# Performance work log

Measured on AMD Instinct MI355X. Metric: run time of the kernel, lower is better.

The kernel has to match this reference:

```python
import jax, jax.numpy as jnp
import numpy as np

B, S, D = 2, 1024, 1024
N_HEADS = 16
R = 128
M = 8
N_NEURONS = 256


def group_gate(gate, n_basis):
    # gate: [B,S,N] -> [B,S,M], sum over consecutive groups, then normalize
    b, s, n = gate.shape
    gs = n // n_basis  # exact by construction (256/8)
    g = gate.reshape(b, s, n_basis, gs).sum(axis=-1)
    return g / (g.sum(axis=-1, keepdims=True) + 1e-8)


def feature_fn(x, neurons, weights):
    # x:[B,S,D], neurons:[M,D,R], weights:[B,S,M] -> h:[B,S,R]
    all_h = jnp.einsum('bsd,mdr->bsmr', x, neurons)
    return jnp.einsum('bsmr,bsm->bsr', all_h, weights)


def restore_fn(h, neurons, weights):
    # h:[B,S,R], neurons:[M,R,D], weights:[B,S,M] -> [B,S,D]
    pre = jnp.einsum('bsr,bsm->bsmr', h, weights)
    return jnp.einsum('bsmr,mrd->bsd', pre, neurons)


def setup_inputs() -> dict:
    key = jax.random.key(0)
    ks = jax.random.split(key, 9)
    sc = 0.02
    return {
        'x': jax.random.normal(ks[0], (B, S, D), jnp.float32),
        'qk_f': jax.random.normal(ks[1], (M, D, R), jnp.float32) * sc,
        'qk_r': jax.random.normal(ks[2], (M, R, D), jnp.float32) * sc,
        'v_f': jax.random.normal(ks[3], (M, D, R), jnp.float32) * sc,
        'v_r': jax.random.normal(ks[4], (M, R, D), jnp.float32) * sc,
        'Wg_q': jax.random.normal(ks[5], (D, N_NEURONS), jnp.float32) * sc,
        'Wg_k': jax.random.normal(ks[6], (D, N_NEURONS), jnp.float32) * sc,
        'Wg_v': jax.random.normal(ks[7], (D, N_NEURONS), jnp.float32) * sc,
        'W_O': jax.random.normal(ks[8], (D, D), jnp.float32) * sc,
    }


def reference(x, qk_f, qk_r, v_f, v_r, Wg_q, Wg_k, Wg_v, W_O):
    # Router gates (softmax over neuron dim), then grouped per basis
    g_Q = jax.nn.softmax(jnp.einsum('bsd,dn->bsn', x, Wg_q), axis=-1)
    g_K = jax.nn.softmax(jnp.einsum('bsd,dn->bsn', x, Wg_k), axis=-1)
    g_V = jax.nn.softmax(jnp.einsum('bsd,dn->bsn', x, Wg_v), axis=-1)
    gQ_b = group_gate(g_Q, M)
    gK_b = group_gate(g_K, M)
    gV_b = group_gate(g_V, M)

    Q = restore_fn(feature_fn(x, qk_f, gQ_b), qk_r, gQ_b)
    K = restore_fn(feature_fn(x, qk_f, gK_b), qk_r, gK_b)
    V = restore_fn(feature_fn(x, v_f, gV_b), v_r, gV_b)

    d_head = D // N_HEADS
    Q = Q.reshape(B, S, N_HEADS, d_head).transpose(0, 2, 1, 3)
    K = K.reshape(B, S, N_HEADS, d_head).transpose(0, 2, 1, 3)
    V = V.reshape(B, S, N_HEADS, d_head).transpose(0, 2, 1, 3)

    scale = jnp.sqrt(jnp.float32(d_head))
    scores = jnp.einsum('bhsd,bhtd->bhst', Q, K) / scale
    causal = jnp.tril(jnp.ones((S, S), dtype=jnp.bool_))
    scores = jnp.where(causal, scores, jnp.finfo(scores.dtype).min)
    attn_w = jax.nn.softmax(scores, axis=-1)
    out = jnp.einsum('bhst,bhtd->bhsd', attn_w, V)
    out = out.transpose(0, 2, 1, 3).reshape(B, S, D)
    out = jnp.einsum('bsd,de->bse', out, W_O)
    return out
```

## Files before the change

### kernel.cpp

```cpp
#include <hip/hip_runtime.h>
#include <hip/hip_bf16.h>

#define BB 2
#define SS 1024
#define DD 1024
#define NH 16
#define DH 64
#define MM 8
#define RR 128
#define NN 256
#define NT (BB*SS)

using bf16 = __hip_bfloat16;

typedef __attribute__((ext_vector_type(8))) short short8;
typedef __attribute__((ext_vector_type(4))) short short4v;
typedef __attribute__((ext_vector_type(4))) float f32x4;

__device__ __forceinline__ void stf(float* p, size_t i, float v) { p[i] = v; }
__device__ __forceinline__ void stf(bf16* p, size_t i, float v) { p[i] = __float2bfloat16(v); }

#define GLD16(g, l) __builtin_amdgcn_global_load_lds( \
    (const __attribute__((address_space(1))) void*)(g), \
    (__attribute__((address_space(3))) void*)(l), 16, 0, 0)

__device__ __forceinline__ short8 lds_load8(const short* p) {
    short4v a = *(const short4v*)p;
    short4v b = *(const short4v*)(p + 4);
    short8 r;
    r[0] = a[0]; r[1] = a[1]; r[2] = a[2]; r[3] = a[3];
    r[4] = b[0]; r[5] = b[1]; r[6] = b[2]; r[7] = b[3];
    return r;
}

template <typename TC>
__device__ __forceinline__ void gemm64_body(
    const bf16* __restrict__ A, const bf16* __restrict__ Bt, TC* __restrict__ C,
    int Kdim, int Nz, int m0, int n0, bf16* As, bf16* Bs) {
    const int tid = threadIdx.x;
    const int wave = tid >> 6, lane = tid & 63;
    const int quad = lane >> 4, l15 = lane & 15;
    const int wr = wave >> 1, wc = wave & 1;

    f32x4 acc[2][4];
#pragma unroll
    for (int i = 0; i < 2; ++i)
#pragma unroll
        for (int j = 0; j < 4; ++j) acc[i][j] = (f32x4)0.f;

    for (int k0 = 0; k0 < Kdim; k0 += 64) {
        __syncthreads();
#pragma unroll
        for (int i = 0; i < 2; ++i) {
            const int L = i * 256 + wave * 64 + lane;
            const int row = L >> 3;
            const int gch = (L & 7) ^ ((row >> 1) & 7);
            GLD16(A + (size_t)(m0 + row) * Kdim + k0 + gch * 8, &As[(i * 256 + wave * 64) * 8]);
        }
#pragma unroll
        for (int i = 0; i < 4; ++i) {
            const int L = i * 256 + wave * 64 + lane;
            const int row = L >> 3;
            const int gch = (L & 7) ^ ((row >> 1) & 7);
            GLD16(Bt + (size_t)(n0 + row) * Kdim + k0 + gch * 8, &Bs[(i * 256 + wave * 64) * 8]);
        }
        __syncthreads();

#pragma unroll
        for (int kk = 0; kk < 2; ++kk) {
            short8 aF[2], bF[4];
#pragma unroll
            for (int bi = 0; bi < 2; ++bi) {
                int m = wr * 32 + bi * 16 + l15;
                int slot = (kk * 4 + quad) ^ ((m >> 1) & 7);
                aF[bi] = *(const short8*)&As[(m * 8 + slot) * 8];
            }
#pragma unroll
            for (int bj = 0; bj < 4; ++bj) {
                int n = wc * 64 + bj * 16 + l15;
                int slot = (kk * 4 + quad) ^ ((n >> 1) & 7);
                bF[bj] = *(const short8*)&Bs[(n * 8 + slot) * 8];
            }
#pragma unroll
            for (int bi = 0; bi < 2; ++bi)
#pragma unroll
                for (int bj = 0; bj < 4; ++bj)
                    acc[bi][bj] = __builtin_amdgcn_mfma_f32_16x16x32_bf16(aF[bi], bF[bj], acc[bi][bj], 0, 0, 0);
        }
    }

#pragma unroll
    for (int bi = 0; bi < 2; ++bi)
#pragma unroll
        for (int bj = 0; bj < 4; ++bj)
#pragma unroll
            for (int r = 0; r < 4; ++r) {
                int row = m0 + wr * 32 + bi * 16 + quad * 4 + r;
                int col = n0 + wc * 64 + bj * 16 + l15;
                stf(C, (size_t)row * Nz + col, acc[bi][bj][r]);
            }
}

struct GemmZ {
    const bf16* A[5];
    const bf16* Bt[5];
    void* C[5];
    int N[5];
};

__global__ __launch_bounds__(256) void mfma_proj(GemmZ P, int Kdim) {
    __shared__ bf16 As[64 * 64];
    __shared__ bf16 Bs[128 * 64];
    const int bidx = blockIdx.x;
    int z, xx, yy;
    if (bidx < 512) { z = bidx >> 8; int r = bidx & 255; yy = r >> 3; xx = r & 7; }
    else { int r = bidx - 512; z = 2 + r / 64; r = r % 64; yy = r >> 1; xx = r & 1; }
    gemm64_body<bf16>(P.A[z], P.Bt[z], (bf16*)P.C[z], Kdim, P.N[z], yy * 64, xx * 128, As, Bs);
}

__global__ __launch_bounds__(256) void mfma_restore(GemmZ P, int Kdim) {
    __shared__ bf16 As[64 * 64];
    __shared__ bf16 Bs[128 * 64];
    const int z = blockIdx.z;
    gemm64_body<bf16>(P.A[z], P.Bt[z], (bf16*)P.C[z], Kdim, P.N[z],
                      blockIdx.y * 64, blockIdx.x * 128, As, Bs);
}

__global__ __launch_bounds__(256) void mfma_gemm_64(
    const bf16* __restrict__ A, const bf16* __restrict__ Bt, float* __restrict__ C,
    int Kdim, int Ndim) {
    __shared__ bf16 As[64 * 64];
    __shared__ bf16 Bs[128 * 64];
    gemm64_body<float>(A, Bt, C, Kdim, Ndim, blockIdx.y * 64, blockIdx.x * 128, As, Bs);
}

struct ConvJobs {
    const float* src[9];
    bf16* dst[9];
    int K[9], R[9], G[9];
    int tEnd[9];
};

__global__ void convert_kernel(ConvJobs J) {
    __shared__ float tile[32][33];
    const int b = blockIdx.x;
    int j = 0;
    while (j < 8 && b >= J.tEnd[j]) ++j;
    const int local = b - (j > 0 ? J.tEnd[j - 1] : 0);
    const float* src = J.src[j];
    bf16* dst = J.dst[j];
    const int tid = threadIdx.x;

    if (J.G[j] == 0) {
        size_t base = (size_t)local * 4096 + (size_t)tid * 16;
        const float4* s4 = (const float4*)(src + base);
        short* d = (short*)(dst + base);
#pragma unroll
        for (int c = 0; c < 4; ++c) {
            float4 v = s4[c];
            short4v o;
            bf16 t0 = __float2bfloat16(v.x); o[0] = *(short*)&t0;
            bf16 t1 = __float2bfloat16(v.y); o[1] = *(short*)&t1;
            bf16 t2 = __float2bfloat16(v.z); o[2] = *(short*)&t2;
            bf16 t3 = __float2bfloat16(v.w); o[3] = *(short*)&t3;
            *(short4v*)(d + c * 4) = o;
        }
    } else {
        const int Kj = J.K[j], Rj = J.R[j];
        const int Rb = Rj >> 5, Kb = Kj >> 5;
        const int perG = Kb * Rb;
        const int g = local / perG;
        const int rem = local - g * perG;
        const int kb = rem / Rb, rb = rem - kb * Rb;
        const int tx = tid & 31, ty0 = tid >> 5;
        const float* s = src + ((size_t)(g * Kj + kb * 32) * Rj) + rb * 32 + tx;
#pragma unroll
        for (int p = 0; p < 4; ++p)
            tile[ty0 + p * 8][tx] = s[(size_t)(ty0 + p * 8) * Rj];
        __syncthreads();
        bf16* dd = dst + ((size_t)(g * Rj + rb * 32) * Kj) + kb * 32 + tx;
#pragma unroll
        for (int p = 0; p < 4; ++p)
            dd[(size_t)(ty0 + p * 8) * Kj] = __float2bfloat16(tile[tx][ty0 + p * 8]);
    }
}

__global__ void gate_combine(const bf16* __restrict__ logitsAll,
                             const bf16* __restrict__ allh,
                             bf16* __restrict__ preQ, bf16* __restrict__ preK,
                             bf16* __restrict__ preV) {
    const int t = blockIdx.x;
    const int n = threadIdx.x;
    const int wave = n >> 6, lane = n & 63;
    __shared__ float wred[3][4];
    __shared__ float sred[3][4];
    __shared__ float gred[3][8];

    float v[3], e[3];
#pragma unroll
    for (int z = 0; z < 3; ++z)
        v[z] = __bfloat162float(logitsAll[(size_t)z * NT * NN + (size_t)t * NN + n]);

    float mz[3];
#pragma unroll
    for (int z = 0; z < 3; ++z) {
        mz[z] = v[z];
#pragma unroll
        for (int off = 1; off <= 32; off <<= 1)
            mz[z] = fmaxf(mz[z], __shfl_xor(mz[z], off));
    }
    if (lane == 0) {
#pragma unroll
        for (int z = 0; z < 3; ++z) wred[z][wave] = mz[z];
    }
    __syncthreads();
    float gmax[3];
#pragma unroll
    for (int z = 0; z < 3; ++z)
        gmax[z] = fmaxf(fmaxf(wred[z][0], wred[z][1]), fmaxf(wred[z][2], wred[z][3]));

    float ws[3];
#pragma unroll
    for (int z = 0; z < 3; ++z) {
        e[z] = __expf(v[z] - gmax[z]);
        ws[z] = e[z];
#pragma unroll
        for (int off = 1; off <= 32; off <<= 1)
            ws[z] += __shfl_xor(ws[z], off);
    }
    if (lane == 0) {
#pragma unroll
        for (int z = 0; z < 3; ++z) sred[z][wave] = ws[z];
    }
    float gs[3];
#pragma unroll
    for (int z = 0; z < 3; ++z) {
        gs[z] = e[z];
#pragma unroll
        for (int off = 1; off <= 16; off <<= 1)
            gs[z] += __shfl_xor(gs[z], off);
    }
    __syncthreads();
    float total[3];
#pragma unroll
    for (int z = 0; z < 3; ++z)
        total[z] = sred[z][0] + sred[z][1] + sred[z][2] + sred[z][3];
    if ((n & 31) == 0) {
#pragma unroll
        for (int z = 0; z < 3; ++z) gred[z][n >> 5] = gs[z] / total[z];
    }
    __syncthreads();

    float gv[3][8];
#pragma unroll
    for (int z = 0; z < 3; ++z) {
        float tot = 0.f;
#pragma unroll
        for (int m = 0; m < 8; ++m) tot += gred[z][m];
        float inv = 1.0f / (tot + 1e-8f);
#pragma unroll
        for (int m = 0; m < 8; ++m) gv[z][m] = gred[z][m] * inv;
    }

    const int r0 = n & 127;
    const int half = n >> 7;
    const bf16* src_qk = allh + (size_t)t * 1024;
    const bf16* src_v  = allh + (size_t)NT * DD + (size_t)t * 1024;
    float hq = 0.f, hk = 0.f, hv = 0.f;
#pragma unroll
    for (int m = 0; m < 8; ++m) {
        float aqk = __bfloat162float(src_qk[m * 128 + r0]);
        float av  = __bfloat162float(src_v[m * 128 + r0]);
        hq += aqk * gv[0][m];
        hk += aqk * gv[1][m];
        hv += av  * gv[2][m];
    }
    __syncthreads();
#pragma unroll
    for (int mm = 0; mm < 4; ++mm) {
        int m = half * 4 + mm;
        size_t o = (size_t)t * 1024 + m * 128 + r0;
        preQ[o] = __float2bfloat16(hq * gv[0][m]);
        preK[o] = __float2bfloat16(hk * gv[1][m]);
        preV[o] = __float2bfloat16(hv * gv[2][m]);
    }
}

#define LDK 68

__global__ __launch_bounds__(256) void flash_attn_causal(
    const bf16* __restrict__ Q, const bf16* __restrict__ K,
    const bf16* __restrict__ V, bf16* __restrict__ out) {
    const int bx = blockIdx.x;
    const int qt = 15 - (bx >> 5);
    const int bh = bx & 31;
    const int b = bh >> 4;
    const int h = bh & 15;
    const int kt_hi = qt + 1;

    const int tid = threadIdx.x;
    const int wave = tid >> 6;
    const int lane = tid & 63;
    const int quad = lane >> 4;
    const int l15 = lane & 15;

    __shared__ short Ks[2][64 * 64];
    __shared__ short Vt[2][64 * LDK];
    __shared__ short Ps[4 * 16 * LDK];

    const int q_row = qt * 64 + wave * 16 + l15;
    const bf16* qptr = Q + (size_t)(b * SS + q_row) * DD + h * DH + quad * 8;
    short8 aq0 = *(const short8*)qptr;
    short8 aq1 = *(const short8*)(qptr + 32);

    const int krp = tid & 31;
    const int dhb = (tid >> 5) * 8;

    float m_r[4], l_r[4];
    f32x4 o[4];
#pragma unroll
    for (int r = 0; r < 4; ++r) { m_r[r] = -3.0e38f; l_r[r] = 0.f; }
#pragma unroll
    for (int cc = 0; cc < 4; ++cc) o[cc] = (f32x4)0.f;

    const float scale = 0.125f;

    {
#pragma unroll
        for (int i = 0; i < 2; ++i) {
            const int L = i * 256 + wave * 64 + lane;
            const int row = L >> 3;
            const int gch = (L & 7) ^ ((row >> 1) & 7);
            GLD16(K + (size_t)(b * SS + row) * DD + h * DH + gch * 8,
                  &Ks[0][(i * 256 + wave * 64) * 8]);
        }
        const bf16* s0 = V + (size_t)(b * SS + 2 * krp) * DD + h * DH + dhb;
        short8 r0 = *(const short8*)s0;
        short8 r1 = *(const short8*)(s0 + DD);
#pragma unroll
        for (int i = 0; i < 8; ++i) {
            unsigned int pk = (unsigned short)r0[i] | ((unsigned int)(unsigned short)r1[i] << 16);
            *(unsigned int*)&Vt[0][(dhb + i) * LDK + 2 * krp] = pk;
        }
        __syncthreads();
    }

    for (int kt = 0; kt < kt_hi; ++kt) {
        const int buf = kt & 1;
        const bool pf = (kt + 1 < kt_hi);
        short8 pr0, pr1;
        if (pf) {
#pragma unroll
            for (int i = 0; i < 2; ++i) {
                const int L = i * 256 + wave * 64 + lane;
                const int row = L >> 3;
                const int gch = (L & 7) ^ ((row >> 1) & 7);
                GLD16(K + (size_t)(b * SS + (kt + 1) * 64 + row) * DD + h * DH + gch * 8,
                      &Ks[buf ^ 1][(i * 256 + wave * 64) * 8]);
            }
            const bf16* s0 = V + (size_t)(b * SS + (kt + 1) * 64 + 2 * krp) * DD + h * DH + dhb;
            pr0 = *(const short8*)s0;
            pr1 = *(const short8*)(s0 + DD);
        }

        const short* KsB = Ks[buf];
        f32x4 s[4];
#pragma unroll
        for (int cc = 0; cc < 4; ++cc) {
            int n = cc * 16 + l15;
            int sl0 = quad ^ ((n >> 1) & 7);
            int sl1 = (quad + 4) ^ ((n >> 1) & 7);
            short8 bk0 = *(const short8*)&KsB[(n * 8 + sl0) * 8];
            short8 bk1 = *(const short8*)&KsB[(n * 8 + sl1) * 8];
            f32x4 acc = (f32x4)0.f;
            acc = __builtin_amdgcn_mfma_f32_16x16x32_bf16(aq0, bk0, acc, 0, 0, 0);
            acc = __builtin_amdgcn_mfma_f32_16x16x32_bf16(aq1, bk1, acc, 0, 0, 0);
            s[cc] = acc;
        }

        const bool diag = (kt == qt);
#pragma unroll
        for (int cc = 0; cc < 4; ++cc) {
#pragma unroll
            for (int r = 0; r < 4; ++r) {
                float v = s[cc][r] * scale;
                if (diag) {
                    int row_rel = wave * 16 + quad * 4 + r;
                    int col_rel = cc * 16 + l15;
                    if (col_rel > row_rel) v = -3.0e38f;
                }
                s[cc][r] = v;
            }
        }

        float p[4][4];
        float alpha[4];
#pragma unroll
        for (int r = 0; r < 4; ++r) {
            float mx = fmaxf(fmaxf(s[0][r], s[1][r]), fmaxf(s[2][r], s[3][r]));
            mx = fmaxf(mx, __shfl_xor(mx, 1));
            mx = fmaxf(mx, __shfl_xor(mx, 2));
            mx = fmaxf(mx, __shfl_xor(mx, 4));
            mx = fmaxf(mx, __shfl_xor(mx, 8));
            float new_m = fmaxf(m_r[r], mx);
            alpha[r] = __expf(m_r[r] - new_m);
            float rs = 0.f;
#pragma unroll
            for (int cc = 0; cc < 4; ++cc) {
                float e = __expf(s[cc][r] - new_m);
                p[cc][r] = e;
                rs += e;
            }
            rs += __shfl_xor(rs, 1);
            rs += __shfl_xor(rs, 2);
            rs += __shfl_xor(rs, 4);
            rs += __shfl_xor(rs, 8);
            l_r[r] = l_r[r] * alpha[r] + rs;
            m_r[r] = new_m;
        }
#pragma unroll
        for (int cc = 0; cc < 4; ++cc)
#pragma unroll
            for (int r = 0; r < 4; ++r) o[cc][r] *= alpha[r];

        short* pw = &Ps[wave * 16 * LDK];
#pragma unroll
        for (int cc = 0; cc < 4; ++cc)
#pragma unroll
            for (int r = 0; r < 4; ++r) {
                bf16 hb = __float2bfloat16(p[cc][r]);
                pw[(quad * 4 + r) * LDK + cc * 16 + l15] = *(short*)&hb;
            }

        short8 ap0 = lds_load8(&pw[l15 * LDK + quad * 8]);
        short8 ap1 = lds_load8(&pw[l15 * LDK + 32 + quad * 8]);

        const short* VtB = Vt[buf];
#pragma unroll
        for (int cc = 0; cc < 4; ++cc) {
            short8 bv0 = lds_load8(&VtB[(cc * 16 + l15) * LDK + quad * 8]);
            short8 bv1 = lds_load8(&VtB[(cc * 16 + l15) * LDK + 32 + quad * 8]);
            o[cc] = __builtin_amdgcn_mfma_f32_16x16x32_bf16(ap0, bv0, o[cc], 0, 0, 0);
            o[cc] = __builtin_amdgcn_mfma_f32_16x16x32_bf16(ap1, bv1, o[cc], 0, 0, 0);
        }

        if (pf) {
#pragma unroll
            for (int i = 0; i < 8; ++i) {
                unsigned int pk = (unsigned short)pr0[i] | ((unsigned int)(unsigned short)pr1[i] << 16);
                *(unsigned int*)&Vt[buf ^ 1][(dhb + i) * LDK + 2 * krp] = pk;
            }
        }
        __syncthreads();
    }

    float inv[4];
#pragma unroll
    for (int r = 0; r < 4; ++r) inv[r] = 1.0f / l_r[r];
#pragma unroll
    for (int cc = 0; cc < 4; ++cc)
#pragma unroll
        for (int r = 0; r < 4; ++r) {
            int row = qt * 64 + wave * 16 + quad * 4 + r;
            out[(size_t)(b * SS + row) * DD + h * DH + cc * 16 + l15] =
                __float2bfloat16(o[cc][r] * inv[r]);
        }
}

extern "C" void kernel_launch(void* const* d_in, const int* in_sizes, int n_in,
                              void* d_out, int out_size, void* d_ws, size_t ws_size,
                              hipStream_t stream) {
    const float* x    = (const float*)d_in[0];
    const float* qk_f = (const float*)d_in[1];
    const float* qk_r = (const float*)d_in[2];
    const float* v_f  = (const float*)d_in[3];
    const float* v_r  = (const float*)d_in[4];
    const float* Wg_q = (const float*)d_in[5];
    const float* Wg_k = (const float*)d_in[6];
    const float* Wg_v = (const float*)d_in[7];
    const float* W_O  = (const float*)d_in[8];

    char* w = (char*)d_ws;
    const size_t MB = 1 << 20;
    bf16* xb     = (bf16*)(w + 0);
    bf16* wg_bt  = (bf16*)(w + 4 * MB);
    bf16* fbt    = (bf16*)(w + (size_t)(5.5 * MB));
    bf16* logits = (bf16*)(w + (size_t)(9.5 * MB));
    bf16* qkr_bt = (bf16*)(w + 16 * MB);
    bf16* vr_bt  = (bf16*)(w + 18 * MB);
    bf16* wo_bt  = (bf16*)(w + 20 * MB);
    bf16* preQ   = (bf16*)(w + 0);
    bf16* preK   = (bf16*)(w + 4 * MB);
    bf16* Kb     = (bf16*)(w + 8 * MB);
    bf16* Vb     = (bf16*)(w + 12 * MB);
    bf16* attnb  = (bf16*)(w + 0);
    bf16* allh   = (bf16*)d_out;
    bf16* preV   = allh + (size_t)NT * DD;
    bf16* Qb     = (bf16*)d_out;
    float* out   = (float*)d_out;

    ConvJobs J;
    J.src[0] = qk_f; J.dst[0] = fbt;              J.K[0] = 1024; J.R[0] = 128;  J.G[0] = 8;
    J.src[1] = v_f;  J.dst[1] = fbt + 1024*1024;  J.K[1] = 1024; J.R[1] = 128;  J.G[1] = 8;
    J.src[2] = qk_r; J.dst[2] = qkr_bt;           J.K[2] = 1024; J.R[2] = 1024; J.G[2] = 1;
    J.src[3] = v_r;  J.dst[3] = vr_bt;            J.K[3] = 1024; J.R[3] = 1024; J.G[3] = 1;
    J.src[4] = W_O;  J.dst[4] = wo_bt;            J.K[4] = 1024; J.R[4] = 1024; J.G[4] = 1;
    J.src[5] = Wg_q; J.dst[5] = wg_bt;            J.K[5] = 1024; J.R[5] = 256;  J.G[5] = 1;
    J.src[6] = Wg_k; J.dst[6] = wg_bt + 256*1024; J.K[6] = 1024; J.R[6] = 256;  J.G[6] = 1;
    J.src[7] = Wg_v; J.dst[7] = wg_bt + 2*256*1024; J.K[7] = 1024; J.R[7] = 256; J.G[7] = 1;
    J.src[8] = x;    J.dst[8] = xb;               J.K[8] = 0;    J.R[8] = 0;    J.G[8] = 0;
    int tiles[9] = {1024, 1024, 1024, 1024, 1024, 256, 256, 256, 512};
    int cum = 0;
    for (int i = 0; i < 9; ++i) { cum += tiles[i]; J.tEnd[i] = cum; }
    convert_kernel<<<cum, 256, 0, stream>>>(J);

    GemmZ Pp;
    Pp.A[0] = Pp.A[1] = Pp.A[2] = Pp.A[3] = Pp.A[4] = xb;
    Pp.Bt[0] = fbt;             Pp.Bt[1] = fbt + 1024*1024;
    Pp.Bt[2] = wg_bt;           Pp.Bt[3] = wg_bt + 256*1024;  Pp.Bt[4] = wg_bt + 2*256*1024;
    Pp.C[0] = allh;             Pp.C[1] = allh + (size_t)NT * DD;
    Pp.C[2] = logits;           Pp.C[3] = logits + (size_t)NT * NN;
    Pp.C[4] = logits + 2 * (size_t)NT * NN;
    Pp.N[0] = 1024; Pp.N[1] = 1024; Pp.N[2] = 256; Pp.N[3] = 256; Pp.N[4] = 256;
    mfma_proj<<<dim3(704), 256, 0, stream>>>(Pp, DD);

    gate_combine<<<NT, 256, 0, stream>>>(logits, allh, preQ, preK, preV);

    GemmZ Pr;
    Pr.A[0] = preQ; Pr.A[1] = preK; Pr.A[2] = preV;
    Pr.Bt[0] = qkr_bt; Pr.Bt[1] = qkr_bt; Pr.Bt[2] = vr_bt;
    Pr.C[0] = Qb; Pr.C[1] = Kb; Pr.C[2] = Vb;
    Pr.N[0] = Pr.N[1] = Pr.N[2] = 1024;
    Pr.A[3] = Pr.A[4] = nullptr; Pr.Bt[3] = Pr.Bt[4] = nullptr;
    Pr.C[3] = Pr.C[4] = nullptr; Pr.N[3] = Pr.N[4] = 0;
    mfma_restore<<<dim3(8, 32, 3), 256, 0, stream>>>(Pr, DD);

    flash_attn_causal<<<dim3(512), 256, 0, stream>>>(Qb, Kb, Vb, attnb);

    mfma_gemm_64<<<dim3(8, 32), 256, 0, stream>>>(attnb, wo_bt, out, DD, DD);
}
```

Baseline: 195.2 us.

## Remap blocks per XCD for L2 locality and skip lazy softmax rescaling

Remaps block indices in all GEMM kernels and flash attention so that consecutive work tiles land on the same XCD (blockIdx & 7 chooses the XCD chunk). The goal is better per-XCD L2 reuse of shared A/B rows and K/V heads. Flash attention also adopts lazy rescaling: the running max and the O/l rescale are updated only when some row's max grows by more than 8, which saves exps and multiplies. This risks larger intermediate exponent values, bounded by e^8, and the causal tile order changes to interleave long and short query tiles.

New measurement: 193.7 us. About the same (-0.7%).

```diff
diff --git a/kernel.cpp b/kernel.cpp
--- a/kernel.cpp
+++ b/kernel.cpp
@@ -111,19 +111,21 @@
 __global__ __launch_bounds__(256) void mfma_proj(GemmZ P, int Kdim) {
     __shared__ bf16 As[64 * 64];
     __shared__ bf16 Bs[128 * 64];
-    const int bidx = blockIdx.x;
+    const int wk = (blockIdx.x & 7) * 88 + (blockIdx.x >> 3);
     int z, xx, yy;
-    if (bidx < 512) { z = bidx >> 8; int r = bidx & 255; yy = r >> 3; xx = r & 7; }
-    else { int r = bidx - 512; z = 2 + r / 64; r = r % 64; yy = r >> 1; xx = r & 1; }
+    if (wk < 512) { z = wk >> 8; int r = wk & 255; yy = r >> 3; xx = r & 7; }
+    else { int r = wk - 512; z = 2 + r / 64; r = r % 64; yy = r >> 1; xx = r & 1; }
     gemm64_body<bf16>(P.A[z], P.Bt[z], (bf16*)P.C[z], Kdim, P.N[z], yy * 64, xx * 128, As, Bs);
 }
 
 __global__ __launch_bounds__(256) void mfma_restore(GemmZ P, int Kdim) {
     __shared__ bf16 As[64 * 64];
     __shared__ bf16 Bs[128 * 64];
-    const int z = blockIdx.z;
+    const int wk = (blockIdx.x & 7) * 96 + (blockIdx.x >> 3);
+    const int z = wk >> 8;
+    const int r = wk & 255;
     gemm64_body<bf16>(P.A[z], P.Bt[z], (bf16*)P.C[z], Kdim, P.N[z],
-                      blockIdx.y * 64, blockIdx.x * 128, As, Bs);
+                      (r >> 3) * 64, (r & 7) * 128, As, Bs);
 }
 
 __global__ __launch_bounds__(256) void mfma_gemm_64(
@@ -131,7 +133,8 @@
     int Kdim, int Ndim) {
     __shared__ bf16 As[64 * 64];
     __shared__ bf16 Bs[128 * 64];
-    gemm64_body<float>(A, Bt, C, Kdim, Ndim, blockIdx.y * 64, blockIdx.x * 128, As, Bs);
+    const int wk = (blockIdx.x & 7) * 32 + (blockIdx.x >> 3);
+    gemm64_body<float>(A, Bt, C, Kdim, Ndim, (wk >> 3) * 64, (wk & 7) * 128, As, Bs);
 }
 
 struct ConvJobs {
@@ -292,8 +295,10 @@
     const bf16* __restrict__ Q, const bf16* __restrict__ K,
     const bf16* __restrict__ V, bf16* __restrict__ out) {
     const int bx = blockIdx.x;
-    const int qt = 15 - (bx >> 5);
-    const int bh = bx & 31;
+    const int xcd = bx & 7, slot = bx >> 3;
+    const int bh = xcd * 4 + (slot & 3);
+    const int qtk = slot >> 2;
+    const int qt = (qtk < 8) ? (15 - qtk) : (qtk - 8);
     const int b = bh >> 4;
     const int h = bh & 15;
     const int kt_hi = qt + 1;
@@ -393,21 +398,37 @@
             }
         }
 
+        float mx[4];
+#pragma unroll
+        for (int r = 0; r < 4; ++r) {
+            float m2 = fmaxf(fmaxf(s[0][r], s[1][r]), fmaxf(s[2][r], s[3][r]));
+            m2 = fmaxf(m2, __shfl_xor(m2, 1));
+            m2 = fmaxf(m2, __shfl_xor(m2, 2));
+            m2 = fmaxf(m2, __shfl_xor(m2, 4));
+            m2 = fmaxf(m2, __shfl_xor(m2, 8));
+            mx[r] = m2;
+        }
+        bool grew = false;
+#pragma unroll
+        for (int r = 0; r < 4; ++r) grew = grew || (mx[r] > m_r[r] + 8.f);
+        float alpha[4];
+        const bool need = __any(grew);
+        if (need) {
+#pragma unroll
+            for (int r = 0; r < 4; ++r) {
+                float nm = fmaxf(m_r[r], mx[r]);
+                alpha[r] = __expf(m_r[r] - nm);
+                m_r[r] = nm;
+            }
+        }
+
         float p[4][4];
-        float alpha[4];
 #pragma unroll
         for (int r = 0; r < 4; ++r) {
-            float mx = fmaxf(fmaxf(s[0][r], s[1][r]), fmaxf(s[2][r], s[3][r]));
-            mx = fmaxf(mx, __shfl_xor(mx, 1));
-            mx = fmaxf(mx, __shfl_xor(mx, 2));
-            mx = fmaxf(mx, __shfl_xor(mx, 4));
-            mx = fmaxf(mx, __shfl_xor(mx, 8));
-            float new_m = fmaxf(m_r[r], mx);
-            alpha[r] = __expf(m_r[r] - new_m);
             float rs = 0.f;
 #pragma unroll
             for (int cc = 0; cc < 4; ++cc) {
-                float e = __expf(s[cc][r] - new_m);
+                float e = __expf(s[cc][r] - m_r[r]);
                 p[cc][r] = e;
                 rs += e;
             }
@@ -415,13 +436,15 @@
             rs += __shfl_xor(rs, 2);
             rs += __shfl_xor(rs, 4);
             rs += __shfl_xor(rs, 8);
-            l_r[r] = l_r[r] * alpha[r] + rs;
-            m_r[r] = new_m;
-        }
-#pragma unroll
-        for (int cc = 0; cc < 4; ++cc)
-#pragma unroll
-            for (int r = 0; r < 4; ++r) o[cc][r] *= alpha[r];
+            if (need) l_r[r] = l_r[r] * alpha[r] + rs;
+            else      l_r[r] += rs;
+        }
+        if (need) {
+#pragma unroll
+            for (int cc = 0; cc < 4; ++cc)
+#pragma unroll
+                for (int r = 0; r < 4; ++r) o[cc][r] *= alpha[r];
+        }
 
         short* pw = &Ps[wave * 16 * LDK];
 #pragma unroll
@@ -533,9 +556,9 @@
     Pr.N[0] = Pr.N[1] = Pr.N[2] = 1024;
     Pr.A[3] = Pr.A[4] = nullptr; Pr.Bt[3] = Pr.Bt[4] = nullptr;
     Pr.C[3] = Pr.C[4] = nullptr; Pr.N[3] = Pr.N[4] = 0;
-    mfma_restore<<<dim3(8, 32, 3), 256, 0, stream>>>(Pr, DD);
+    mfma_restore<<<dim3(768), 256, 0, stream>>>(Pr, DD);
 
     flash_attn_causal<<<dim3(512), 256, 0, stream>>>(Qb, Kb, Vb, attnb);
 
-    mfma_gemm_64<<<dim3(8, 32), 256, 0, stream>>>(attnb, wo_bt, out, DD, DD);
-}
+    mfma_gemm_64<<<dim3(256), 256, 0, stream>>>(attnb, wo_bt, out, DD, DD);
+}
```
